# Performance work log

Measured on AMD Instinct MI355X. Metric: run time of the kernel, lower is better.

Reference implementation:

```python
import jax, jax.numpy as jnp
import numpy as np

HIDDEN = 2048
NH = 32
NKV = 8
HD = HIDDEN // NH  # 64
GROUP = NH // NKV  # 4


def setup_inputs() -> dict:
    key = jax.random.key(0)
    ks = jax.random.split(key, 9)
    s = 1.0 / np.sqrt(HIDDEN)
    x = jax.random.normal(ks[0], (2, 2048, HIDDEN), dtype=jnp.float32)
    Wq = jax.random.uniform(ks[1], (HIDDEN, HIDDEN), jnp.float32, -s, s)
    bq = jax.random.uniform(ks[2], (HIDDEN,), jnp.float32, -s, s)
    Wk = jax.random.uniform(ks[3], (HIDDEN, NKV * HD), jnp.float32, -s, s)
    bk = jax.random.uniform(ks[4], (NKV * HD,), jnp.float32, -s, s)
    Wv = jax.random.uniform(ks[5], (HIDDEN, NKV * HD), jnp.float32, -s, s)
    bv = jax.random.uniform(ks[6], (NKV * HD,), jnp.float32, -s, s)
    Wo = jax.random.uniform(ks[7], (HIDDEN, HIDDEN), jnp.float32, -s, s)
    bo = jax.random.uniform(ks[8], (HIDDEN,), jnp.float32, -s, s)
    return {"x": x, "Wq": Wq, "bq": bq, "Wk": Wk, "bk": bk,
            "Wv": Wv, "bv": bv, "Wo": Wo, "bo": bo}


def reference(x, Wq, bq, Wk, bk, Wv, bv, Wo, bo):
    B, S, D = x.shape
    scale = 1.0 / np.sqrt(HD).astype(np.float32)
    q = (x @ Wq + bq).reshape(B, S, NH, HD).transpose(0, 2, 1, 3)   # [B,H,S,hd]
    k = (x @ Wk + bk).reshape(B, S, NKV, HD).transpose(0, 2, 1, 3)  # [B,KV,S,hd]
    v = (x @ Wv + bv).reshape(B, S, NKV, HD).transpose(0, 2, 1, 3)
    # repeat_interleave KV heads: kv head j serves query heads j*GROUP..(j+1)*GROUP-1
    k = jnp.repeat(k, GROUP, axis=1)  # [B,H,S,hd]
    v = jnp.repeat(v, GROUP, axis=1)
    scores = jnp.einsum('bhqd,bhkd->bhqk', q, k) * scale  # [B,H,S,S]
    w = jax.nn.softmax(scores, axis=-1)
    out = jnp.einsum('bhqk,bhkd->bhqd', w, v)              # [B,H,S,hd]
    out = out.transpose(0, 2, 1, 3).reshape(B, S, D)
    return out @ Wo + bo
```

## Files before the change

kernel.cpp:

```cpp
#include <hip/hip_runtime.h>

#define HID 2048
#define SEQ 2048
#define NH_ 32
#define NKV_ 8
#define HD_ 64

typedef __attribute__((ext_vector_type(8))) short s8v;
typedef __attribute__((ext_vector_type(4))) short s4v;
typedef __attribute__((ext_vector_type(4))) float f4v;
typedef __attribute__((ext_vector_type(4))) unsigned int u4v;
typedef unsigned int u32;
typedef unsigned short u16;

#define QSCALE 0.18033688011112042f

__device__ __forceinline__ u16 f2bf(float f) {
  u32 u = __builtin_bit_cast(u32, f);
  u = u + 0x7FFFu + ((u >> 16) & 1u);
  return (u16)(u >> 16);
}

__device__ __forceinline__ float hw_exp2(float x) {
  float r;
  asm("v_exp_f32 %0, %1" : "=v"(r) : "v"(x));
  return r;
}

__device__ __forceinline__ void gl_lds16(const void* g, void* l) {
  __builtin_amdgcn_global_load_lds((const __attribute__((address_space(1))) u32*)g,
                                   (__attribute__((address_space(3))) u32*)l, 16, 0, 0);
}

__global__ __launch_bounds__(256) void cast_bf16_k(const float* __restrict__ in,
                                                   u16* __restrict__ out, int n) {
  int i = (blockIdx.x * 256 + threadIdx.x) * 4;
  if (i >= n) return;
  const float4 v = *reinterpret_cast<const float4*>(in + i);
  ushort4 o;
  o.x = f2bf(v.x); o.y = f2bf(v.y); o.z = f2bf(v.z); o.w = f2bf(v.w);
  *reinterpret_cast<ushort4*>(out + i) = o;
}

__global__ __launch_bounds__(256) void transp_bf16_k(const float* __restrict__ W,
                                                     u16* __restrict__ Wt, int K, int N) {
  __shared__ float t[64][65];
  const int n0 = blockIdx.x * 64, k0 = blockIdx.y * 64;
  const int tid = threadIdx.x;
  const int tr = tid >> 4, tc = tid & 15;
#pragma unroll
  for (int i = 0; i < 4; ++i) {
    int r = i * 16 + tr;
    const float4 v = *reinterpret_cast<const float4*>(&W[(size_t)(k0 + r) * N + n0 + tc * 4]);
    t[r][tc * 4 + 0] = v.x; t[r][tc * 4 + 1] = v.y;
    t[r][tc * 4 + 2] = v.z; t[r][tc * 4 + 3] = v.w;
  }
  __syncthreads();
#pragma unroll
  for (int i = 0; i < 4; ++i) {
    int r = i * 16 + tr;
    ushort4 o;
    o.x = f2bf(t[tc * 4 + 0][r]); o.y = f2bf(t[tc * 4 + 1][r]);
    o.z = f2bf(t[tc * 4 + 2][r]); o.w = f2bf(t[tc * 4 + 3][r]);
    *reinterpret_cast<ushort4*>(&Wt[(size_t)(n0 + r) * K + k0 + tc * 4]) = o;
  }
}

template <int MODE>
__global__ __launch_bounds__(256) void gemm_k(const u16* __restrict__ A,
                                              const u16* __restrict__ Bt,
                                              const float* __restrict__ b0,
                                              const float* __restrict__ b1,
                                              const float* __restrict__ b2,
                                              void* __restrict__ o0,
                                              void* __restrict__ o1,
                                              void* __restrict__ o2,
                                              int M, int N, int K) {
  __shared__ u16 As[128 * 64];
  __shared__ u16 Bs[128 * 64];
  const int tid = threadIdx.x;
  const int w = tid >> 6, l = tid & 63;
  const int wr = w >> 1, wc = w & 1;
  const int lr = l & 15, lg = l >> 4;
  const int m0 = blockIdx.y * 128, n0 = blockIdx.x * 128;
  f4v acc[4][4] = {};
  for (int k0 = 0; k0 < K; k0 += 64) {
#pragma unroll
    for (int i = 0; i < 4; ++i) {
      int c = i * 256 + tid;
      int r = c >> 3, p = c & 7;
      gl_lds16(&A[(size_t)(m0 + r) * K + k0 + ((p ^ (r & 7)) * 8)], &As[c * 8]);
      gl_lds16(&Bt[(size_t)(n0 + r) * K + k0 + ((p ^ (r & 7)) * 8)], &Bs[c * 8]);
    }
    __syncthreads();
#pragma unroll
    for (int kc = 0; kc < 2; ++kc) {
      s8v af[4], bf[4];
#pragma unroll
      for (int m = 0; m < 4; ++m)
        af[m] = *reinterpret_cast<const s8v*>(
            &As[(wr * 64 + m * 16 + lr) * 64 + ((((kc << 2) + lg) ^ (lr & 7)) << 3)]);
#pragma unroll
      for (int n = 0; n < 4; ++n)
        bf[n] = *reinterpret_cast<const s8v*>(
            &Bs[(wc * 64 + n * 16 + lr) * 64 + ((((kc << 2) + lg) ^ (lr & 7)) << 3)]);
#pragma unroll
      for (int m = 0; m < 4; ++m)
#pragma unroll
        for (int n = 0; n < 4; ++n)
          acc[m][n] = __builtin_amdgcn_mfma_f32_16x16x32_bf16(af[m], bf[n], acc[m][n], 0, 0, 0);
    }
    __syncthreads();
  }
#pragma unroll
  for (int n = 0; n < 4; ++n) {
    const int col = n0 + wc * 64 + n * 16 + lr;
    float bb, scl = 1.0f;
    if (MODE == 2) {
      bb = b0[col];
    } else {
      if (col < 2048) { bb = b0[col]; scl = QSCALE; }
      else if (col < 2560) { bb = b1[col - 2048]; }
      else { bb = b2[col - 2560]; }
    }
#pragma unroll
    for (int m = 0; m < 4; ++m) {
#pragma unroll
      for (int r = 0; r < 4; ++r) {
        const int row = m0 + wr * 64 + m * 16 + lg * 4 + r;
        const float v = (acc[m][n][r] + bb) * scl;
        if (MODE == 2) {
          ((float*)o0)[(size_t)row * N + col] = v;
        } else {
          const int b = row >> 11, s = row & (SEQ - 1);
          if (col < 2048) {
            const int h = col >> 6, d = col & 63;
            ((u16*)o0)[((((size_t)b * NH_ + h) * SEQ + s) << 6) + d] = f2bf(v);
          } else if (col < 2560) {
            const int kv = (col - 2048) >> 6, d = (col - 2048) & 63;
            ((u16*)o1)[((((size_t)b * NKV_ + kv) * SEQ + s) << 6) + d] = f2bf(v);
          } else {
            const int kv = (col - 2560) >> 6, d = (col - 2560) & 63;
            ((u16*)o2)[(((size_t)b * NKV_ + kv) * HD_ + d) * SEQ + s] = f2bf(v);
          }
        }
      }
    }
  }
}

__global__ __launch_bounds__(256) void attn_k(const u16* __restrict__ Q,
                                              const u16* __restrict__ Kg,
                                              const u16* __restrict__ Vt,
                                              u16* __restrict__ Og) {
  __shared__ u16 Ks[128 * 64];
  __shared__ u16 Vs[64 * 128];
  const int tid = threadIdx.x;
  const int w = tid >> 6, l = tid & 63;
  const int lr = l & 15, lg = l >> 4;
  const int qt = blockIdx.x, h = blockIdx.y, b = blockIdx.z;
  const int kvh = h >> 2;
  const u16* Qp = Q + ((((size_t)b * NH_ + h) * SEQ + qt * 128) << 6);
  const u16* Kp = Kg + (((size_t)b * NKV_ + kvh) * SEQ << 6);
  const u16* Vp = Vt + ((size_t)b * NKV_ + kvh) * HD_ * SEQ;

  s8v qf[2][2];
#pragma unroll
  for (int i = 0; i < 2; ++i)
#pragma unroll
    for (int kc = 0; kc < 2; ++kc)
      qf[i][kc] = *reinterpret_cast<const s8v*>(
          &Qp[(w * 32 + i * 16 + lr) * 64 + kc * 32 + lg * 8]);

  float msm[2];
  float lo_[2][4];
  f4v Oacc[2][4] = {};
#pragma unroll
  for (int i = 0; i < 2; ++i) {
    msm[i] = -__builtin_inff();
#pragma unroll
    for (int r = 0; r < 4; ++r) lo_[i][r] = 0.f;
  }

#define STAGE_K(KT)                                                              \
  {                                                                              \
    _Pragma("unroll") for (int i_ = 0; i_ < 4; ++i_) {                           \
      int c_ = i_ * 256 + tid;                                                   \
      int r_ = c_ >> 3, p_ = c_ & 7;                                             \
      gl_lds16(&Kp[((size_t)((KT) * 128 + r_)) * 64 + ((p_ ^ (r_ & 7)) * 8)],    \
               &Ks[c_ * 8]);                                                     \
    }                                                                            \
  }
#define STAGE_V(KT)                                                              \
  {                                                                              \
    _Pragma("unroll") for (int i_ = 0; i_ < 4; ++i_) {                           \
      int c_ = i_ * 256 + tid;                                                   \
      int r_ = c_ >> 4, p_ = c_ & 15;                                            \
      gl_lds16(&Vp[(size_t)r_ * SEQ + (KT) * 128 + ((p_ ^ (r_ & 15)) * 8)],      \
               &Vs[c_ * 8]);                                                     \
    }                                                                            \
  }

  STAGE_K(0);
  STAGE_V(0);
  __syncthreads();

  const int NT = SEQ / 128;
  for (int kt = 0; kt < NT; ++kt) {
    f4v sc[2][8] = {};
#pragma unroll
    for (int kb = 0; kb < 8; ++kb) {
      const int rk = kb * 16 + lr;
#pragma unroll
      for (int kc = 0; kc < 2; ++kc) {
        s8v kfr = *reinterpret_cast<const s8v*>(
            &Ks[rk * 64 + ((((kc << 2) + lg) ^ (lr & 7)) << 3)]);
#pragma unroll
        for (int i = 0; i < 2; ++i)
          sc[i][kb] = __builtin_amdgcn_mfma_f32_16x16x32_bf16(kfr, qf[i][kc], sc[i][kb], 0, 0, 0);
      }
    }

    float fsm[2];
#pragma unroll
    for (int i = 0; i < 2; ++i) {
      float t[8];
#pragma unroll
      for (int kb = 0; kb < 8; ++kb)
        t[kb] = fmaxf(fmaxf(sc[i][kb][0], sc[i][kb][1]),
                      fmaxf(sc[i][kb][2], sc[i][kb][3]));
      float v = fmaxf(fmaxf(fmaxf(t[0], t[1]), fmaxf(t[2], t[3])),
                      fmaxf(fmaxf(t[4], t[5]), fmaxf(t[6], t[7])));
      v = fmaxf(v, __shfl_xor(v, 16));
      v = fmaxf(v, __shfl_xor(v, 32));
      const float mn = fmaxf(msm[i], v);
      fsm[i] = hw_exp2(msm[i] - mn);
      msm[i] = mn;
    }

    __syncthreads();
    if (kt + 1 < NT) STAGE_K(kt + 1);

    float ps[2];
#pragma unroll
    for (int i = 0; i < 2; ++i) {
      float s = 0.f;
#pragma unroll
      for (int kb = 0; kb < 8; ++kb)
#pragma unroll
        for (int r = 0; r < 4; ++r) {
          const float e = hw_exp2(sc[i][kb][r] - msm[i]);
          sc[i][kb][r] = e;
          s += e;
        }
      s += __shfl_xor(s, 16);
      s += __shfl_xor(s, 32);
      ps[i] = s;
    }

#pragma unroll
    for (int i = 0; i < 2; ++i)
#pragma unroll
      for (int r = 0; r < 4; ++r) {
        const float f = __shfl(fsm[i], (lg << 2) + r);
        const float p = __shfl(ps[i], (lg << 2) + r);
        lo_[i][r] = lo_[i][r] * f + p;
#pragma unroll
        for (int df = 0; df < 4; ++df) Oacc[i][df][r] *= f;
      }

#pragma unroll
    for (int c = 0; c < 4; ++c) {
      s8v pa[2];
#pragma unroll
      for (int i = 0; i < 2; ++i) {
        u32 d0, d1, d2, d3;
        asm("v_cvt_pk_bf16_f32 %0, %1, %2" : "=v"(d0) : "v"(sc[i][2 * c][0]), "v"(sc[i][2 * c][1]));
        asm("v_cvt_pk_bf16_f32 %0, %1, %2" : "=v"(d1) : "v"(sc[i][2 * c][2]), "v"(sc[i][2 * c][3]));
        asm("v_cvt_pk_bf16_f32 %0, %1, %2" : "=v"(d2) : "v"(sc[i][2 * c + 1][0]), "v"(sc[i][2 * c + 1][1]));
        asm("v_cvt_pk_bf16_f32 %0, %1, %2" : "=v"(d3) : "v"(sc[i][2 * c + 1][2]), "v"(sc[i][2 * c + 1][3]));
        u4v t = {d0, d1, d2, d3};
        pa[i] = __builtin_bit_cast(s8v, t);
      }
#pragma unroll
      for (int df = 0; df < 4; ++df) {
        const int d = df * 16 + lr;
        const int ch1 = ((c << 2) + (lg >> 1)) ^ lr;
        const int ch2 = ((c << 2) + 2 + (lg >> 1)) ^ lr;
        const s4v v1 = *reinterpret_cast<const s4v*>(&Vs[d * 128 + (ch1 << 3) + ((lg & 1) << 2)]);
        const s4v v2 = *reinterpret_cast<const s4v*>(&Vs[d * 128 + (ch2 << 3) + ((lg & 1) << 2)]);
        const s8v vb = __builtin_shufflevector(v1, v2, 0, 1, 2, 3, 4, 5, 6, 7);
#pragma unroll
        for (int i = 0; i < 2; ++i)
          Oacc[i][df] = __builtin_amdgcn_mfma_f32_16x16x32_bf16(pa[i], vb, Oacc[i][df], 0, 0, 0);
      }
    }

    __syncthreads();
    if (kt + 1 < NT) STAGE_V(kt + 1);
  }

  const int sbase = qt * 128 + w * 32;
#pragma unroll
  for (int i = 0; i < 2; ++i)
#pragma unroll
    for (int df = 0; df < 4; ++df)
#pragma unroll
      for (int r = 0; r < 4; ++r) {
        const int srow = sbase + i * 16 + lg * 4 + r;
        const float v = Oacc[i][df][r] / lo_[i][r];
        Og[((size_t)b * SEQ + srow) * HID + h * 64 + df * 16 + lr] = f2bf(v);
      }
#undef STAGE_K
#undef STAGE_V
}

extern "C" void kernel_launch(void* const* d_in, const int* in_sizes, int n_in,
                              void* d_out, int out_size, void* d_ws, size_t ws_size,
                              hipStream_t stream) {
  (void)in_sizes; (void)n_in; (void)out_size;
  const float* x  = (const float*)d_in[0];
  const float* Wq = (const float*)d_in[1];
  const float* bq = (const float*)d_in[2];
  const float* Wk = (const float*)d_in[3];
  const float* bk = (const float*)d_in[4];
  const float* Wv = (const float*)d_in[5];
  const float* bv = (const float*)d_in[6];
  const float* Wo = (const float*)d_in[7];
  const float* bo = (const float*)d_in[8];
  float* out = (float*)d_out;

  u16* ws    = (u16*)d_ws;
  u16* xb    = ws;
  u16* wqkvt = xb + 8388608;
  u16* wot   = wqkvt + 6291456;
  u16* qb    = wot + 4194304;
  u16* kbuf  = qb + 8388608;
  u16* vtb   = kbuf + 2097152;
  u16* ab    = vtb + 2097152;
  if (ws_size < (size_t)(8388608 + 6291456 + 4194304 + 8388608 + 2097152 +
                         2097152 + 8388608) * 2) return;

  cast_bf16_k<<<8192, 256, 0, stream>>>(x, xb, 8388608);
  transp_bf16_k<<<dim3(32, 32), 256, 0, stream>>>(Wq, wqkvt, 2048, 2048);
  transp_bf16_k<<<dim3(8, 32), 256, 0, stream>>>(Wk, wqkvt + (size_t)2048 * 2048, 2048, 512);
  transp_bf16_k<<<dim3(8, 32), 256, 0, stream>>>(Wv, wqkvt + (size_t)2560 * 2048, 2048, 512);
  transp_bf16_k<<<dim3(32, 32), 256, 0, stream>>>(Wo, wot, 2048, 2048);

  gemm_k<3><<<dim3(24, 32), 256, 0, stream>>>(xb, wqkvt, bq, bk, bv,
                                              qb, kbuf, vtb, 4096, 3072, 2048);

  attn_k<<<dim3(16, 32, 2), 256, 0, stream>>>(qb, kbuf, vtb, ab);

  gemm_k<2><<<dim3(16, 32), 256, 0, stream>>>(ab, wot, bo, nullptr, nullptr,
                                              out, nullptr, nullptr, 4096, 2048, 2048);
}
```

Baseline: 253.3 us.

## Merge prep kernels into one launch and permute V layout for 16-byte loads

Folds the x cast and the four weight transpose/cast launches into one prep kernel that dispatches on block index, removing four kernel launches and their gaps. It also writes V^T with a permuted sequence index inside each 32-element group, so the attention PV loop reads one 8-element vector per fragment instead of two 4-element reads plus a shuffle. The permutation must match the k ordering of the P fragments exactly, otherwise the attention output is wrong. The merged prep kernel now declares shared memory in every block, including the cast blocks that never use it.

```diff
diff --git a/kernel.cpp b/kernel.cpp
--- a/kernel.cpp
+++ b/kernel.cpp
@@ -7,7 +7,6 @@
 #define HD_ 64
 
 typedef __attribute__((ext_vector_type(8))) short s8v;
-typedef __attribute__((ext_vector_type(4))) short s4v;
 typedef __attribute__((ext_vector_type(4))) float f4v;
 typedef __attribute__((ext_vector_type(4))) unsigned int u4v;
 typedef unsigned int u32;
@@ -32,21 +31,11 @@
                                    (__attribute__((address_space(3))) u32*)l, 16, 0, 0);
 }
 
-__global__ __launch_bounds__(256) void cast_bf16_k(const float* __restrict__ in,
-                                                   u16* __restrict__ out, int n) {
-  int i = (blockIdx.x * 256 + threadIdx.x) * 4;
-  if (i >= n) return;
-  const float4 v = *reinterpret_cast<const float4*>(in + i);
-  ushort4 o;
-  o.x = f2bf(v.x); o.y = f2bf(v.y); o.z = f2bf(v.z); o.w = f2bf(v.w);
-  *reinterpret_cast<ushort4*>(out + i) = o;
-}
-
-__global__ __launch_bounds__(256) void transp_bf16_k(const float* __restrict__ W,
-                                                     u16* __restrict__ Wt, int K, int N) {
+__device__ __forceinline__ void transp_body(const float* __restrict__ W,
+                                            u16* __restrict__ Wt, int K, int N,
+                                            int bx, int by, int tid) {
   __shared__ float t[64][65];
-  const int n0 = blockIdx.x * 64, k0 = blockIdx.y * 64;
-  const int tid = threadIdx.x;
+  const int n0 = bx * 64, k0 = by * 64;
   const int tr = tid >> 4, tc = tid & 15;
 #pragma unroll
   for (int i = 0; i < 4; ++i) {
@@ -63,6 +52,36 @@
     o.x = f2bf(t[tc * 4 + 0][r]); o.y = f2bf(t[tc * 4 + 1][r]);
     o.z = f2bf(t[tc * 4 + 2][r]); o.w = f2bf(t[tc * 4 + 3][r]);
     *reinterpret_cast<ushort4*>(&Wt[(size_t)(n0 + r) * K + k0 + tc * 4]) = o;
+  }
+}
+
+__global__ __launch_bounds__(256) void prep_k(const float* __restrict__ x,
+                                              const float* __restrict__ Wq,
+                                              const float* __restrict__ Wk,
+                                              const float* __restrict__ Wv,
+                                              const float* __restrict__ Wo,
+                                              u16* __restrict__ xb,
+                                              u16* __restrict__ wqkvt,
+                                              u16* __restrict__ wot) {
+  const int bid = blockIdx.x, tid = threadIdx.x;
+  if (bid < 8192) {
+    const int i = (bid * 256 + tid) * 4;
+    const float4 v = *reinterpret_cast<const float4*>(x + i);
+    ushort4 o;
+    o.x = f2bf(v.x); o.y = f2bf(v.y); o.z = f2bf(v.z); o.w = f2bf(v.w);
+    *reinterpret_cast<ushort4*>(xb + i) = o;
+  } else if (bid < 8192 + 1024) {
+    const int b2 = bid - 8192;
+    transp_body(Wq, wqkvt, 2048, 2048, b2 & 31, b2 >> 5, tid);
+  } else if (bid < 8192 + 1024 + 256) {
+    const int b2 = bid - (8192 + 1024);
+    transp_body(Wk, wqkvt + (size_t)2048 * 2048, 2048, 512, b2 & 7, b2 >> 3, tid);
+  } else if (bid < 8192 + 1024 + 512) {
+    const int b2 = bid - (8192 + 1024 + 256);
+    transp_body(Wv, wqkvt + (size_t)2560 * 2048, 2048, 512, b2 & 7, b2 >> 3, tid);
+  } else {
+    const int b2 = bid - (8192 + 1024 + 512);
+    transp_body(Wo, wot, 2048, 2048, b2 & 31, b2 >> 5, tid);
   }
 }
 
@@ -141,7 +160,8 @@
             ((u16*)o1)[((((size_t)b * NKV_ + kv) * SEQ + s) << 6) + d] = f2bf(v);
           } else {
             const int kv = (col - 2560) >> 6, d = (col - 2560) & 63;
-            ((u16*)o2)[(((size_t)b * NKV_ + kv) * HD_ + d) * SEQ + s] = f2bf(v);
+            const int sp = (s & ~31) | (((s >> 2) & 3) << 3) | (((s >> 4) & 1) << 2) | (s & 3);
+            ((u16*)o2)[(((size_t)b * NKV_ + kv) * HD_ + d) * SEQ + sp] = f2bf(v);
           }
         }
       }
@@ -285,11 +305,8 @@
 #pragma unroll
       for (int df = 0; df < 4; ++df) {
         const int d = df * 16 + lr;
-        const int ch1 = ((c << 2) + (lg >> 1)) ^ lr;
-        const int ch2 = ((c << 2) + 2 + (lg >> 1)) ^ lr;
-        const s4v v1 = *reinterpret_cast<const s4v*>(&Vs[d * 128 + (ch1 << 3) + ((lg & 1) << 2)]);
-        const s4v v2 = *reinterpret_cast<const s4v*>(&Vs[d * 128 + (ch2 << 3) + ((lg & 1) << 2)]);
-        const s8v vb = __builtin_shufflevector(v1, v2, 0, 1, 2, 3, 4, 5, 6, 7);
+        const int ch = ((c << 2) + lg) ^ lr;
+        const s8v vb = *reinterpret_cast<const s8v*>(&Vs[d * 128 + (ch << 3)]);
 #pragma unroll
         for (int i = 0; i < 2; ++i)
           Oacc[i][df] = __builtin_amdgcn_mfma_f32_16x16x32_bf16(pa[i], vb, Oacc[i][df], 0, 0, 0);
@@ -341,11 +358,7 @@
   if (ws_size < (size_t)(8388608 + 6291456 + 4194304 + 8388608 + 2097152 +
                          2097152 + 8388608) * 2) return;
 
-  cast_bf16_k<<<8192, 256, 0, stream>>>(x, xb, 8388608);
-  transp_bf16_k<<<dim3(32, 32), 256, 0, stream>>>(Wq, wqkvt, 2048, 2048);
-  transp_bf16_k<<<dim3(8, 32), 256, 0, stream>>>(Wk, wqkvt + (size_t)2048 * 2048, 2048, 512);
-  transp_bf16_k<<<dim3(8, 32), 256, 0, stream>>>(Wv, wqkvt + (size_t)2560 * 2048, 2048, 512);
-  transp_bf16_k<<<dim3(32, 32), 256, 0, stream>>>(Wo, wot, 2048, 2048);
+  prep_k<<<10752, 256, 0, stream>>>(x, Wq, Wk, Wv, Wo, xb, wqkvt, wot);
 
   gemm_k<3><<<dim3(24, 32), 256, 0, stream>>>(xb, wqkvt, bq, bk, bv,
                                               qb, kbuf, vtb, 4096, 3072, 2048);
```

New measurement: 239.5 us. 1.06x faster.
